# Kernel optimization log

Hardware: AMD Instinct MI355X
Metric: run time of the kernel (lower is better)

Reference implementation:

```python
import jax, jax.numpy as jnp
import numpy as np

B, S, D, H, HZ = 4096, 64, 9, 128, 32
DT = 0.1


def _lstm_cell(x, h, c, Wih, Whh, bih, bhh):
    gates = x @ Wih.T + bih + h @ Whh.T + bhh
    i, f, g, o = jnp.split(gates, 4, axis=-1)
    c_new = jax.nn.sigmoid(f) * c + jax.nn.sigmoid(i) * jnp.tanh(g)
    h_new = jax.nn.sigmoid(o) * jnp.tanh(c_new)
    return h_new, c_new


def _forward(input_batch, W_ih_enc, W_hh_enc, b_ih_enc, b_hh_enc, W_e, V_e, v_e,
             W_d, V_d, v_d, W_ih_dec, W_hh_dec, b_ih_dec, b_hh_dec,
             W_out, b_out, scaler_mean, scaler_std, pos_mean):
    bsz = input_batch.shape[0]
    # ---- encoder with input attention ----
    x_perm = jnp.swapaxes(input_batch, 1, 2)          # (B, D, S)
    attn_input = jnp.einsum('bds,ts->bdt', x_perm, V_e)  # V_e * x^i, precomputed once
    h0 = jnp.zeros((bsz, H), input_batch.dtype)
    c0 = jnp.zeros((bsz, H), input_batch.dtype)

    def enc_step(carry, x_t):
        h, c = carry
        attn_hidden = jnp.concatenate([h, c], axis=1) @ W_e.T          # (B, S)
        comb = jnp.tanh(attn_hidden[:, None, :] + attn_input)          # (B, D, S)
        e = comb @ v_e                                                 # (B, D)
        alpha = jax.nn.softmax(e, axis=1)
        h, c = _lstm_cell(alpha * x_t, h, c, W_ih_enc, W_hh_enc, b_ih_enc, b_hh_enc)
        return (h, c), h

    (h_enc, c_enc), hs = jax.lax.scan(enc_step, (h0, c0), jnp.swapaxes(input_batch, 0, 1))
    enc_hidden = jnp.swapaxes(hs, 0, 1)               # (B, S, H)
    attn_encoder = enc_hidden @ V_d.T                 # V_d * h_j, precomputed once

    # ---- initial physics state ----
    pos = input_batch[:, -1, :3] + pos_mean
    vel = input_batch[:, -1, 3:6] * scaler_std + scaler_mean
    pre_vel = input_batch[:, -2, 3:6] * scaler_std + scaler_mean
    acc = (vel - pre_vel) / DT

    def dec_step(carry, _):
        d, c, pos, vel, acc = carry
        attn_dec = jnp.concatenate([d, c], axis=1) @ W_d.T             # (B, H)
        comb = jnp.tanh(attn_dec[:, None, :] + attn_encoder)           # (B, S, H)
        beta = jax.nn.softmax(comb @ v_d, axis=1)                      # (B, S)
        context = jnp.einsum('bs,bsh->bh', beta, enc_hidden)           # (B, H)
        phys = jnp.concatenate([pos - pos_mean,
                                (vel - scaler_mean) / scaler_std,
                                acc / scaler_std], axis=1)             # (B, 9)
        d, c = _lstm_cell(jnp.concatenate([phys, context], axis=1), d, c,
                          W_ih_dec, W_hh_dec, b_ih_dec, b_hh_dec)
        pred_acc = (jnp.concatenate([d, context], axis=1) @ W_out.T + b_out) * scaler_std
        pos_pred = pos + vel * DT + 0.5 * acc * DT * DT                # Verlet position
        vel_new = vel + 0.5 * (acc + pred_acc) * DT                    # Verlet velocity
        out = jnp.concatenate([pos_pred, vel_new, pred_acc], axis=1)   # (B, 9)
        return (d, c, pos_pred, vel_new, pred_acc), out

    _, outs = jax.lax.scan(dec_step, (h_enc, c_enc, pos, vel, acc), None, length=HZ)
    return jnp.swapaxes(outs, 0, 1)                   # (B, HZ, 9)


def setup_inputs() -> dict:
    key = jax.random.key(0)
    ks = jax.random.split(key, 16)
    p = lambda k, shape, s=0.05: jax.random.normal(k, shape, dtype=jnp.float32) * s
    return dict(
        input_batch=jax.random.normal(ks[0], (B, S, D), dtype=jnp.float32),
        W_ih_enc=p(ks[1], (4 * H, D)), W_hh_enc=p(ks[2], (4 * H, H)),
        b_ih_enc=jnp.zeros((4 * H,), jnp.float32), b_hh_enc=jnp.zeros((4 * H,), jnp.float32),
        W_e=p(ks[3], (S, 2 * H)), V_e=p(ks[4], (S, S)), v_e=p(ks[5], (S,)),
        W_d=p(ks[6], (H, 2 * H)), V_d=p(ks[7], (H, H)), v_d=p(ks[8], (H,)),
        W_ih_dec=p(ks[9], (4 * H, 9 + H)), W_hh_dec=p(ks[10], (4 * H, H)),
        b_ih_dec=jnp.zeros((4 * H,), jnp.float32), b_hh_dec=jnp.zeros((4 * H,), jnp.float32),
        W_out=p(ks[11], (3, 2 * H)), b_out=jnp.zeros((3,), jnp.float32),
        scaler_mean=p(ks[12], (3,), 0.1),
        scaler_std=jnp.abs(p(ks[13], (3,), 0.1)) + 1.0,
        pos_mean=p(ks[14], (3,), 0.1),
    )


def reference(input_batch, W_ih_enc, W_hh_enc, b_ih_enc, b_hh_enc, W_e, V_e, v_e,
              W_d, V_d, v_d, W_ih_dec, W_hh_dec, b_ih_dec, b_hh_dec,
              W_out, b_out, scaler_mean, scaler_std, pos_mean):
    return _forward(input_batch, W_ih_enc, W_hh_enc, b_ih_enc, b_hh_enc, W_e, V_e, v_e,
                    W_d, V_d, v_d, W_ih_dec, W_hh_dec, b_ih_dec, b_hh_dec,
                    W_out, b_out, scaler_mean, scaler_std, pos_mean)
```

## Files before the change

### kernel.cpp

```cpp
#include <hip/hip_runtime.h>
#include <hip/hip_bf16.h>
#include <hip/hip_fp8.h>

#define B_   4096
#define S_   64
#define D_   9
#define H_   128
#define HZ_  32
#define DT_  0.1f

#define OFF_WET    0
#define OFF_VET    16384
#define OFF_WENCT  20480
#define OFF_BENC   90624
#define OFF_WDT    91136
#define OFF_WDECT  123904
#define OFF_BDEC   259584
#define OFF_WOUTT  260096
#define OFF_VDT    260864
#define OFF_DECD   277248
#define OFF_DECC   801536
#define F32_TOTAL  1325824
#define PREP_N     277248

#define DCX_S   552
#define OF_D0   0
#define OF_D1   128
#define OF_C    256
#define OF_CTX  384
#define OF_PH   512

typedef __bf16 bf16x8 __attribute__((ext_vector_type(8)));
typedef float  f32x4  __attribute__((ext_vector_type(4)));
typedef float  f32x2  __attribute__((ext_vector_type(2)));

__device__ __forceinline__ float fast_tanh(float x) {
    float e = __expf(2.0f * x);
    return 1.0f - __fdividef(2.0f, e + 1.0f);
}
__device__ __forceinline__ float sigf(float x) {
    return __fdividef(1.0f, 1.0f + __expf(-x));
}
__device__ __forceinline__ float bf_lo(unsigned int u) { return __uint_as_float(u << 16); }
__device__ __forceinline__ float bf_hi(unsigned int u) { return __uint_as_float(u & 0xffff0000u); }
__device__ __forceinline__ float bfu2f(unsigned short u) { return __uint_as_float((unsigned int)u << 16); }
__device__ __forceinline__ unsigned short f2bfu(float f) {
    __hip_bfloat16 b = __float2bfloat16(f);
    return *(unsigned short*)&b;
}
__device__ __forceinline__ unsigned int pack_bf(float lo, float hi) {
    return (unsigned int)f2bfu(lo) | ((unsigned int)f2bfu(hi) << 16);
}
__device__ __forceinline__ float f8tof(unsigned int byte) {
    __hip_fp8_e4m3 t; t.__x = (unsigned char)byte; return (float)t;
}
__device__ __forceinline__ unsigned char f2f8(float f) {
    __hip_fp8_e4m3 q(f); return q.__x;
}
__device__ __forceinline__ unsigned int pack4_f8(float a, float b, float c, float d) {
    return (unsigned int)f2f8(a) | ((unsigned int)f2f8(b) << 8) |
           ((unsigned int)f2f8(c) << 16) | ((unsigned int)f2f8(d) << 24);
}
template<bool HI>
__device__ __forceinline__ f32x2 cvt2f8(unsigned int u) {
    return __builtin_amdgcn_cvt_pk_f32_fp8(u, HI);
}

__global__ void prep_kernel(const float* __restrict__ Wih_e, const float* __restrict__ Whh_e,
    const float* __restrict__ bih_e, const float* __restrict__ bhh_e,
    const float* __restrict__ W_e, const float* __restrict__ V_e,
    const float* __restrict__ W_d, const float* __restrict__ V_d,
    const float* __restrict__ Wih_d, const float* __restrict__ Whh_d,
    const float* __restrict__ bih_d, const float* __restrict__ bhh_d,
    const float* __restrict__ W_out, float* __restrict__ ws) {
  for (int idx = blockIdx.x * blockDim.x + threadIdx.x; idx < PREP_N;
       idx += gridDim.x * blockDim.x) {
    int i = idx;
    if (i < 16384) { continue; }
    i -= 16384;
    if (i < 4096) { int s = i >> 6, t = i & 63; ws[OFF_VET + i] = V_e[t * 64 + s]; continue; }
    i -= 4096;
    if (i < 70144) { continue; }
    i -= 70144;
    if (i < 512) { ws[OFF_BENC + i] = bih_e[i] + bhh_e[i]; continue; }
    i -= 512;
    if (i < 32768) { continue; }
    i -= 32768;
    if (i < 135680) { continue; }
    i -= 135680;
    if (i < 512) { ws[OFF_BDEC + i] = bih_d[i] + bhh_d[i]; continue; }
    i -= 512;
    if (i < 768) { int k = i / 3, j = i % 3; ws[OFF_WOUTT + i] = W_out[j * 256 + k]; continue; }
  }
}

__global__ void prep_mfma_kernel(const float* __restrict__ W_d,
    const float* __restrict__ Wih_d, const float* __restrict__ Whh_d,
    unsigned short* __restrict__ WdTm, unsigned short* __restrict__ WdecTm) {
  int idx = blockIdx.x * blockDim.x + threadIdx.x;
  if (idx < 32768) {
    int j = idx & 7, l = (idx >> 3) & 63, t = idx >> 9;
    int nt = t & 7, ks = t >> 3;
    int k = ks * 32 + (l >> 4) * 8 + j;
    int n = nt * 16 + (l & 15);
    WdTm[idx] = f2bfu(W_d[n * 256 + k]);
    return;
  }
  int i2 = idx - 32768;
  if (i2 < 147456) {
    int j = i2 & 7, l = (i2 >> 3) & 63, t = i2 >> 9;
    int ks = t % 9, tile = t / 9;
    int q = tile & 3, is = tile >> 2;
    int k = ks * 32 + (l >> 4) * 8 + j;
    int g = q * 128 + is * 16 + (l & 15);
    float v;
    if (k < 128)      v = Whh_d[g * 128 + k];
    else if (k < 256) v = Wih_d[g * 137 + 9 + (k - 128)];
    else if (k < 265) v = Wih_d[g * 137 + (k - 256)];
    else              v = 0.f;
    WdecTm[i2] = f2bfu(v);
  }
}

__global__ void prep_enc_mfma_kernel(const float* __restrict__ W_e,
    const float* __restrict__ Wih_e, const float* __restrict__ Whh_e,
    const float* __restrict__ V_d,
    unsigned short* __restrict__ WeTm, unsigned short* __restrict__ WencTm,
    unsigned short* __restrict__ VdTm) {
  int idx = blockIdx.x * blockDim.x + threadIdx.x;
  if (idx < 16384) {
    int j = idx & 7, l = (idx >> 3) & 63, tile = idx >> 9;
    int nt = tile & 3, ks = tile >> 2;
    int k = ks * 32 + (l >> 4) * 8 + j;
    int n = nt * 16 + (l & 15);
    WeTm[idx] = f2bfu(W_e[n * 256 + k]);
    return;
  }
  int i2 = idx - 16384;
  if (i2 < 81920) {
    int j = i2 & 7, l = (i2 >> 3) & 63, tile = i2 >> 9;
    int ks = tile % 5, tq = tile / 5;
    int q = tq & 3, is = tq >> 2;
    int kk = (l >> 4) * 8 + j;
    int g = q * 128 + is * 16 + (l & 15);
    float v;
    if (ks < 4) v = Whh_e[g * 128 + ks * 32 + kk];
    else        v = (kk < 9) ? Wih_e[g * 9 + kk] : 0.f;
    WencTm[i2] = f2bfu(v);
    return;
  }
  int i3 = i2 - 81920;
  if (i3 < 16384) {
    int j = i3 & 7, l = (i3 >> 3) & 63, tile = i3 >> 9;
    int nt = tile & 7, ks = tile >> 3;
    int i = ks * 32 + (l >> 4) * 8 + j;
    int n = nt * 16 + (l & 15);
    VdTm[i3] = f2bfu(V_d[n * 128 + i]);
  }
}

__global__ __launch_bounds__(512, 1) void encoder_mfma_kernel(
    const float* __restrict__ x_in, const float* __restrict__ ws,
    const float* __restrict__ v_e_g,
    const unsigned short* __restrict__ WeTm, const unsigned short* __restrict__ WencTm,
    __hip_bfloat16* __restrict__ EH,
    unsigned short* __restrict__ dG, float* __restrict__ cG) {
  __shared__ unsigned short hA[2][16 * 296];
  __shared__ float cF[16 * 132];
  __shared__ float ahL[16 * 64];
  __shared__ unsigned short aiL[16 * 576];
  __shared__ unsigned short xbL[16 * 576];

  const int tid = threadIdx.x;
  const int b0 = blockIdx.x * 16;
  const int l = tid & 63, w = tid >> 6;
  const int quad = l >> 4, l15 = l & 15;

  for (int i = tid; i < 16 * 576; i += 512) {
    int m = i / 576, r = i % 576;
    xbL[i] = f2bfu(x_in[(size_t)(b0 + m) * 576 + r]);
  }
  for (int i = tid; i < 2 * 16 * 296; i += 512) ((unsigned short*)hA)[i] = 0;
  for (int i = tid; i < 16 * 132; i += 512) cF[i] = 0.f;
  __syncthreads();

  {
    const float* __restrict__ VeT = ws + OFF_VET;
    for (int i = tid; i < 16 * 576; i += 512) {
      int t = i & 63, dd = (i >> 6) % 9, m = i / 576;
      float acc = 0.f;
      for (int s = 0; s < 64; ++s) acc += bfu2f(xbL[m * 576 + s * 9 + dd]) * VeT[s * 64 + t];
      aiL[m * 576 + dd * 64 + t] = f2bfu(acc);
    }
  }
  const float ve_r = v_e_g[l];
  const int ig = w * 16 + l15;
  float bbq[4];
  #pragma unroll
  for (int q = 0; q < 4; ++q) bbq[q] = ws[OFF_BENC + q * 128 + ig];
  __syncthreads();

  for (int t = 0; t < S_; ++t) {
    unsigned short* bufC = hA[t & 1];
    unsigned short* bufN = hA[(t + 1) & 1];
    if (w < 4) {
      f32x4 acc = {0.f, 0.f, 0.f, 0.f};
      #pragma unroll
      for (int ks = 0; ks < 8; ++ks) {
        uint4 au = *(const uint4*)&bufC[l15 * 296 + ks * 32 + quad * 8];
        uint4 bu = *(const uint4*)(WeTm + (size_t)((ks * 4 + w) * 64 + l) * 8);
        acc = __builtin_amdgcn_mfma_f32_16x16x32_bf16(
            __builtin_bit_cast(bf16x8, au), __builtin_bit_cast(bf16x8, bu), acc, 0, 0, 0);
      }
      #pragma unroll
      for (int r = 0; r < 4; ++r)
        ahL[(quad * 4 + r) * 64 + w * 16 + l15] = acc[r];
    }
    __syncthreads();
    {
      const int m0 = 2 * w, m1 = 2 * w + 1;
      float a0 = ahL[m0 * 64 + l], a1 = ahL[m1 * 64 + l];
      float e0k = -1e30f, e1k = -1e30f;
      #pragma unroll
      for (int dd = 0; dd < 9; ++dd) {
        float t0 = fast_tanh(a0 + bfu2f(aiL[m0 * 576 + dd * 64 + l])) * ve_r;
        float t1 = fast_tanh(a1 + bfu2f(aiL[m1 * 576 + dd * 64 + l])) * ve_r;
        #pragma unroll
        for (int off = 32; off; off >>= 1) {
          t0 += __shfl_xor(t0, off, 64);
          t1 += __shfl_xor(t1, off, 64);
        }
        if (l == dd) { e0k = t0; e1k = t1; }
      }
      float mx0 = e0k, mx1 = e1k;
      #pragma unroll
      for (int off = 8; off; off >>= 1) {
        mx0 = fmaxf(mx0, __shfl_xor(mx0, off, 64));
        mx1 = fmaxf(mx1, __shfl_xor(mx1, off, 64));
      }
      float ex0 = (l < 9) ? __expf(e0k - mx0) : 0.f;
      float ex1 = (l < 9) ? __expf(e1k - mx1) : 0.f;
      float s0 = ex0, s1 = ex1;
      #pragma unroll
      for (int off = 8; off; off >>= 1) {
        s0 += __shfl_xor(s0, off, 64);
        s1 += __shfl_xor(s1, off, 64);
      }
      if (l < 9) {
        bufC[m0 * 296 + 256 + l] = f2bfu(__fdividef(ex0, s0) * bfu2f(xbL[m0 * 576 + t * 9 + l]));
        bufC[m1 * 296 + 256 + l] = f2bfu(__fdividef(ex1, s1) * bfu2f(xbL[m1 * 576 + t * 9 + l]));
      }
    }
    __syncthreads();
    {
      uint4 af[5];
      #pragma unroll
      for (int ks = 0; ks < 4; ++ks)
        af[ks] = *(const uint4*)&bufC[l15 * 296 + ks * 32 + quad * 8];
      af[4] = *(const uint4*)&bufC[l15 * 296 + 256 + quad * 8];
      f32x4 g4[4];
      #pragma unroll
      for (int q = 0; q < 4; ++q) {
        f32x4 acc = {0.f, 0.f, 0.f, 0.f};
        #pragma unroll
        for (int ks = 0; ks < 5; ++ks) {
          uint4 bu = *(const uint4*)(WencTm + (size_t)(((w * 4 + q) * 5 + ks) * 64 + l) * 8);
          acc = __builtin_amdgcn_mfma_f32_16x16x32_bf16(
              __builtin_bit_cast(bf16x8, af[ks]), __builtin_bit_cast(bf16x8, bu), acc, 0, 0, 0);
        }
        g4[q] = acc;
      }
      #pragma unroll
      for (int r = 0; r < 4; ++r) {
        int m = quad * 4 + r;
        float gi = g4[0][r] + bbq[0];
        float gf = g4[1][r] + bbq[1];
        float gg = g4[2][r] + bbq[2];
        float go = g4[3][r] + bbq[3];
        float co = cF[m * 132 + ig];
        float cn = sigf(gf) * co + sigf(gi) * fast_tanh(gg);
        float hn = sigf(go) * fast_tanh(cn);
        cF[m * 132 + ig] = cn;
        bufN[m * 296 + ig] = f2bfu(hn);
        bufN[m * 296 + 128 + ig] = f2bfu(cn);
        EH[((size_t)(b0 + m) * S_ + t) * H_ + ig] = __float2bfloat16(hn);
      }
    }
    __syncthreads();
  }
  for (int i = tid; i < 16 * 128; i += 512) {
    int m = i >> 7, ii = i & 127;
    dG[(size_t)(b0 + m) * 128 + ii] = hA[0][m * 296 + ii];
    cG[(size_t)(b0 + m) * 128 + ii] = cF[m * 132 + ii];
  }
}

__global__ __launch_bounds__(256) void attnenc_mfma_kernel(
    const unsigned short* __restrict__ EH, const unsigned short* __restrict__ VdTm,
    unsigned char* __restrict__ AETf8, unsigned char* __restrict__ EHf8) {
  const int tid = threadIdx.x;
  const int b = blockIdx.x * 4 + (tid >> 6);
  const int l = tid & 63;
  const int quad = l >> 4, l15 = l & 15;

  const unsigned short* ehb = EH + (size_t)b * 8192;
  uint4 A[4][4];
  #pragma unroll
  for (int st = 0; st < 4; ++st)
    #pragma unroll
    for (int ks = 0; ks < 4; ++ks)
      A[st][ks] = *(const uint4*)(ehb + (st * 16 + l15) * 128 + ks * 32 + quad * 8);

  {
    unsigned char* e8b = EHf8 + (size_t)b * 8192;
    #pragma unroll
    for (int st = 0; st < 4; ++st)
      #pragma unroll
      for (int ks = 0; ks < 4; ++ks) {
        uint4 a = A[st][ks];
        uint2 pk;
        pk.x = pack4_f8(bf_lo(a.x), bf_hi(a.x), bf_lo(a.y), bf_hi(a.y));
        pk.y = pack4_f8(bf_lo(a.z), bf_hi(a.z), bf_lo(a.w), bf_hi(a.w));
        *(uint2*)(e8b + (st * 16 + l15) * 128 + ks * 32 + quad * 8) = pk;
      }
  }

  unsigned char* outb = AETf8 + (size_t)b * 8192;
  const int k = l15;
  #pragma unroll
  for (int nt = 0; nt < 8; ++nt) {
    uint4 Bf[4];
    #pragma unroll
    for (int ks = 0; ks < 4; ++ks)
      Bf[ks] = *(const uint4*)(VdTm + (size_t)((ks * 8 + nt) * 64 + l) * 8);
    int kg = nt * 16 + k;
    int kb = kg >> 3, k7 = kg & 7;
    #pragma unroll
    for (int st = 0; st < 4; ++st) {
      f32x4 acc = {0.f, 0.f, 0.f, 0.f};
      #pragma unroll
      for (int ks = 0; ks < 4; ++ks)
        acc = __builtin_amdgcn_mfma_f32_16x16x32_bf16(
            __builtin_bit_cast(bf16x8, A[st][ks]), __builtin_bit_cast(bf16x8, Bf[ks]), acc, 0, 0, 0);
      #pragma unroll
      for (int r = 0; r < 4; ++r) {
        int s = st * 16 + quad * 4 + r;
        outb[kb * 512 + s * 8 + k7] = f2f8(acc[r]);
      }
    }
  }
}

__global__ __launch_bounds__(512, 2) void dec_fused_kernel(
    const float* __restrict__ ws,
    const unsigned char* __restrict__ AETf8, const unsigned char* __restrict__ EHf8,
    const unsigned short* __restrict__ dG, const float* __restrict__ cG,
    const unsigned short* __restrict__ WdTm, const unsigned short* __restrict__ WdecTm,
    const float* __restrict__ v_d_g, const float* __restrict__ b_out_g,
    const float* __restrict__ smean_g, const float* __restrict__ sstd_g,
    const float* __restrict__ pmean_g,
    const float* __restrict__ x_in,
    float* __restrict__ out) {
  __shared__ unsigned char  AET[8][8192];
  __shared__ unsigned char  EHL[8][8192];
  __shared__ unsigned short dcx[16 * DCX_S];
  __shared__ unsigned short adL[8 * 128];
  __shared__ float          bet[8][64];
  __shared__ float          vdL[128];
  __shared__ float          pcs[8 * 3 * 8];
  __shared__ float          pvs[8 * 12];

  const int tid = threadIdx.x;
  const int b0 = blockIdx.x * 8;
  const int l = tid & 63, w = tid >> 6;
  const int quad = l >> 4, l15 = l & 15;
  const int i = w * 16 + l15;

  for (int idx = tid; idx < 16 * DCX_S; idx += 512) dcx[idx] = 0;
  {
    const uint4* srcA = (const uint4*)(AETf8 + (size_t)b0 * 8192);
    const uint4* srcE = (const uint4*)(EHf8 + (size_t)b0 * 8192);
    uint4* dstA = (uint4*)AET;
    uint4* dstE = (uint4*)EHL;
    for (int idx = tid; idx < 4096; idx += 512) {
      dstA[idx] = srcA[idx];
      dstE[idx] = srcE[idx];
    }
  }
  if (tid < 128) vdL[tid] = v_d_g[tid];
  __syncthreads();

  if (tid < 128) {
    int m = tid >> 4, i0 = (tid & 15) * 8;
    uint4 dv = *(const uint4*)(dG + (size_t)(b0 + m) * 128 + i0);
    *(uint4*)&dcx[m * DCX_S + OF_D0 + i0] = dv;
    float4 c0 = *(const float4*)(cG + (size_t)(b0 + m) * 128 + i0);
    float4 c1 = *(const float4*)(cG + (size_t)(b0 + m) * 128 + i0 + 4);
    uint4 pk;
    pk.x = pack_bf(c0.x, c0.y); pk.y = pack_bf(c0.z, c0.w);
    pk.z = pack_bf(c1.x, c1.y); pk.w = pack_bf(c1.z, c1.w);
    *(uint4*)&dcx[m * DCX_S + OF_C + i0] = pk;
  }
  if (tid < 24) {
    int m = tid / 3, jj = tid % 3;
    const float* xi = x_in + (size_t)(b0 + m) * 576;
    float sm = smean_g[jj], ss = sstd_g[jj], pm = pmean_g[jj];
    float v  = xi[63 * 9 + 3 + jj] * ss + sm;
    float pv = xi[62 * 9 + 3 + jj] * ss + sm;
    float pos = xi[63 * 9 + jj] + pm;
    float ac = (v - pv) / DT_;
    float* P = pvs + m * 12;
    P[jj] = pos; P[3 + jj] = v; P[6 + jj] = ac;
    dcx[m * DCX_S + OF_PH + jj]     = f2bfu(pos - pm);
    dcx[m * DCX_S + OF_PH + 3 + jj] = f2bfu((v - sm) / ss);
    dcx[m * DCX_S + OF_PH + 6 + jj] = f2bfu(ac / ss);
  }
  float bb[4];
  #pragma unroll
  for (int q = 0; q < 4; ++q) bb[q] = ws[OFF_BDEC + q * 128 + i];
  float k_sm = 0.f, k_ss = 1.f, k_pm = 0.f, k_bo = 0.f;
  if (tid < 24) {
    int jj = tid % 3;
    k_sm = smean_g[jj]; k_ss = sstd_g[jj]; k_pm = pmean_g[jj]; k_bo = b_out_g[jj];
  }
  float cReg[4];
  #pragma unroll
  for (int r = 0; r < 4; ++r)
    cReg[r] = (quad < 2) ? cG[(size_t)(b0 + quad * 4 + r) * 128 + i] : 0.f;
  __syncthreads();

  {
    const int nt = w;
    f32x4 acc = {0.f, 0.f, 0.f, 0.f};
    #pragma unroll
    for (int ks = 0; ks < 8; ++ks) {
      int off = (ks < 4) ? (OF_D0 + ks * 32) : (OF_C + (ks - 4) * 32);
      uint4 au = *(const uint4*)&dcx[l15 * DCX_S + off + quad * 8];
      uint4 bu = *(const uint4*)(WdTm + (size_t)((ks * 8 + nt) * 64 + l) * 8);
      acc = __builtin_amdgcn_mfma_f32_16x16x32_bf16(
          __builtin_bit_cast(bf16x8, au), __builtin_bit_cast(bf16x8, bu), acc, 0, 0, 0);
    }
    if (quad < 2) {
      int n = nt * 16 + l15;
      #pragma unroll
      for (int r = 0; r < 4; ++r) adL[(quad * 4 + r) * 128 + n] = f2bfu(acc[r]);
    }
  }
  __syncthreads();

  for (int hz = 0; hz < HZ_; ++hz) {
    const int dcur = (hz & 1) ? OF_D1 : OF_D0;
    const int dnxt = (hz & 1) ? OF_D0 : OF_D1;

    {
      const unsigned char* aet = AET[w];
      const unsigned short* adp = adL + w * 128;
      float eacc[4] = {0.f, 0.f, 0.f, 0.f};
      #pragma unroll
      for (int kb = 0; kb < 16; ++kb) {
        uint2 av = *(const uint2*)(aet + kb * 512 + l * 8);
        uint4 ad8 = *(const uint4*)(adp + kb * 8);
        float4 v0 = *(const float4*)&vdL[kb * 8];
        float4 v1 = *(const float4*)&vdL[kb * 8 + 4];
        f32x2 p0 = cvt2f8<false>(av.x), p1 = cvt2f8<true>(av.x);
        f32x2 p2 = cvt2f8<false>(av.y), p3 = cvt2f8<true>(av.y);
        float e = eacc[kb & 3];
        e += fast_tanh(bf_lo(ad8.x) + p0[0]) * v0.x;
        e += fast_tanh(bf_hi(ad8.x) + p0[1]) * v0.y;
        e += fast_tanh(bf_lo(ad8.y) + p1[0]) * v0.z;
        e += fast_tanh(bf_hi(ad8.y) + p1[1]) * v0.w;
        e += fast_tanh(bf_lo(ad8.z) + p2[0]) * v1.x;
        e += fast_tanh(bf_hi(ad8.z) + p2[1]) * v1.y;
        e += fast_tanh(bf_lo(ad8.w) + p3[0]) * v1.z;
        e += fast_tanh(bf_hi(ad8.w) + p3[1]) * v1.w;
        eacc[kb & 3] = e;
      }
      float e0 = (eacc[0] + eacc[1]) + (eacc[2] + eacc[3]);
      float mx = e0;
      #pragma unroll
      for (int off = 32; off; off >>= 1) mx = fmaxf(mx, __shfl_xor(mx, off, 64));
      float ex = __expf(e0 - mx);
      float ss = ex;
      #pragma unroll
      for (int off = 32; off; off >>= 1) ss += __shfl_xor(ss, off, 64);
      bet[w][l] = __fdividef(ex, ss);
    }
    {
      const unsigned char* ehb = EHL[w];
      const int i0 = l15 * 8;
      float a[8];
      #pragma unroll
      for (int r = 0; r < 8; ++r) a[r] = 0.f;
      #pragma unroll
      for (int it = 0; it < 16; ++it) {
        int s = quad * 16 + it;
        uint2 ev = *(const uint2*)(ehb + s * 128 + i0);
        float bt = bet[w][s];
        f32x2 c0 = cvt2f8<false>(ev.x), c1 = cvt2f8<true>(ev.x);
        f32x2 c2 = cvt2f8<false>(ev.y), c3 = cvt2f8<true>(ev.y);
        a[0] += bt * c0[0]; a[1] += bt * c0[1];
        a[2] += bt * c1[0]; a[3] += bt * c1[1];
        a[4] += bt * c2[0]; a[5] += bt * c2[1];
        a[6] += bt * c3[0]; a[7] += bt * c3[1];
      }
      #pragma unroll
      for (int r = 0; r < 8; ++r) {
        a[r] += __shfl_xor(a[r], 16, 64);
        a[r] += __shfl_xor(a[r], 32, 64);
      }
      if (quad == 0) {
        uint4 pk;
        pk.x = pack_bf(a[0], a[1]); pk.y = pack_bf(a[2], a[3]);
        pk.z = pack_bf(a[4], a[5]); pk.w = pack_bf(a[6], a[7]);
        *(uint4*)&dcx[w * DCX_S + OF_CTX + i0] = pk;
      }
    }
    __syncthreads();

    {
      f32x4 g4[4];
      #pragma unroll
      for (int q = 0; q < 4; ++q) g4[q] = (f32x4){0.f, 0.f, 0.f, 0.f};
      #pragma unroll
      for (int ks = 0; ks < 9; ++ks) {
        int off = (ks < 4) ? (dcur + ks * 32)
                           : ((ks < 8) ? (OF_CTX + (ks - 4) * 32) : OF_PH);
        uint4 af = *(const uint4*)&dcx[l15 * DCX_S + off + quad * 8];
        #pragma unroll
        for (int q = 0; q < 4; ++q) {
          uint4 bu = *(const uint4*)(WdecTm + (size_t)(((w * 4 + q) * 9 + ks) * 64 + l) * 8);
          g4[q] = __builtin_amdgcn_mfma_f32_16x16x32_bf16(
              __builtin_bit_cast(bf16x8, af), __builtin_bit_cast(bf16x8, bu), g4[q], 0, 0, 0);
        }
      }
      if (quad < 2) {
        #pragma unroll
        for (int r = 0; r < 4; ++r) {
          int m = quad * 4 + r;
          float gi = g4[0][r] + bb[0];
          float gf = g4[1][r] + bb[1];
          float gg = g4[2][r] + bb[2];
          float go = g4[3][r] + bb[3];
          float cn = sigf(gf) * cReg[r] + sigf(gi) * fast_tanh(gg);
          float hn = sigf(go) * fast_tanh(cn);
          cReg[r] = cn;
          dcx[m * DCX_S + dnxt + i] = f2bfu(hn);
          dcx[m * DCX_S + OF_C + i] = f2bfu(cn);
        }
      }
    }
    __syncthreads();

    {
      const int nt = w;
      f32x4 acc = {0.f, 0.f, 0.f, 0.f};
      #pragma unroll
      for (int ks = 0; ks < 8; ++ks) {
        int off = (ks < 4) ? (dnxt + ks * 32) : (OF_C + (ks - 4) * 32);
        uint4 au = *(const uint4*)&dcx[l15 * DCX_S + off + quad * 8];
        uint4 bu = *(const uint4*)(WdTm + (size_t)((ks * 8 + nt) * 64 + l) * 8);
        acc = __builtin_amdgcn_mfma_f32_16x16x32_bf16(
            __builtin_bit_cast(bf16x8, au), __builtin_bit_cast(bf16x8, bu), acc, 0, 0, 0);
      }
      if (quad < 2) {
        int n = nt * 16 + l15;
        #pragma unroll
        for (int r = 0; r < 4; ++r) adL[(quad * 4 + r) * 128 + n] = f2bfu(acc[r]);
      }
    }
    if (tid < 192) {
      int m = tid / 24, r2 = tid % 24, jj = r2 >> 3, part = r2 & 7;
      int kbase = (part < 4) ? (dnxt + part * 32) : (OF_CTX + (part - 4) * 32);
      float acc = 0.f;
      #pragma unroll 4
      for (int kk = 0; kk < 32; ++kk)
        acc += bfu2f(dcx[m * DCX_S + kbase + kk]) * ws[OFF_WOUTT + (part * 32 + kk) * 3 + jj];
      pcs[(m * 3 + jj) * 8 + part] = acc;
    }
    __syncthreads();

    if (tid < 24) {
      int m = tid / 3, jj = tid % 3;
      float s = k_bo;
      #pragma unroll
      for (int p = 0; p < 8; ++p) s += pcs[(m * 3 + jj) * 8 + p];
      float pacc = s * k_ss;
      float* P = pvs + m * 12;
      float pos = P[jj], vel = P[3 + jj], ac = P[6 + jj];
      float ppred = pos + vel * DT_ + 0.5f * ac * DT_ * DT_;
      float vnew  = vel + 0.5f * (ac + pacc) * DT_;
      size_t ob = ((size_t)(b0 + m) * HZ_ + hz) * 9;
      out[ob + jj] = ppred; out[ob + 3 + jj] = vnew; out[ob + 6 + jj] = pacc;
      P[jj] = ppred; P[3 + jj] = vnew; P[6 + jj] = pacc;
      dcx[m * DCX_S + OF_PH + jj]     = f2bfu(ppred - k_pm);
      dcx[m * DCX_S + OF_PH + 3 + jj] = f2bfu((vnew - k_sm) / k_ss);
      dcx[m * DCX_S + OF_PH + 6 + jj] = f2bfu(pacc / k_ss);
    }
  }
}

extern "C" void kernel_launch(void* const* d_in, const int* in_sizes, int n_in,
                              void* d_out, int out_size, void* d_ws, size_t ws_size,
                              hipStream_t stream) {
  (void)in_sizes; (void)n_in; (void)out_size; (void)ws_size;
  const float* x      = (const float*)d_in[0];
  const float* Wih_e  = (const float*)d_in[1];
  const float* Whh_e  = (const float*)d_in[2];
  const float* bih_e  = (const float*)d_in[3];
  const float* bhh_e  = (const float*)d_in[4];
  const float* W_e    = (const float*)d_in[5];
  const float* V_e    = (const float*)d_in[6];
  const float* v_e    = (const float*)d_in[7];
  const float* W_d    = (const float*)d_in[8];
  const float* V_d    = (const float*)d_in[9];
  const float* v_d    = (const float*)d_in[10];
  const float* Wih_d  = (const float*)d_in[11];
  const float* Whh_d  = (const float*)d_in[12];
  const float* bih_d  = (const float*)d_in[13];
  const float* bhh_d  = (const float*)d_in[14];
  const float* W_out  = (const float*)d_in[15];
  const float* b_out  = (const float*)d_in[16];
  const float* smean  = (const float*)d_in[17];
  const float* sstd   = (const float*)d_in[18];
  const float* pmean  = (const float*)d_in[19];

  float* ws = (float*)d_ws;
  unsigned short* WeTm   = (unsigned short*)(ws + OFF_WET);
  unsigned short* WencTm = (unsigned short*)(ws + OFF_WENCT);
  unsigned short* WdTm   = (unsigned short*)(ws + OFF_WDT);
  unsigned short* WdecTm = (unsigned short*)(ws + OFF_WDECT);
  unsigned short* VdTm   = (unsigned short*)(ws + OFF_VDT);
  unsigned short* dG     = (unsigned short*)(ws + OFF_DECD);
  float* cG = ws + OFF_DECC;
  unsigned short* ub  = (unsigned short*)(ws + F32_TOTAL);
  unsigned short* EH  = ub;
  unsigned char*  AETf8 = (unsigned char*)(ub + 33554432);
  unsigned char*  EHf8  = AETf8 + (size_t)B_ * 8192;
  float* out = (float*)d_out;

  prep_kernel<<<(PREP_N + 255) / 256, 256, 0, stream>>>(
      Wih_e, Whh_e, bih_e, bhh_e, W_e, V_e, W_d, V_d,
      Wih_d, Whh_d, bih_d, bhh_d, W_out, ws);
  prep_mfma_kernel<<<(32768 + 147456 + 255) / 256, 256, 0, stream>>>(
      W_d, Wih_d, Whh_d, WdTm, WdecTm);
  prep_enc_mfma_kernel<<<(16384 + 81920 + 16384 + 255) / 256, 256, 0, stream>>>(
      W_e, Wih_e, Whh_e, V_d, WeTm, WencTm, VdTm);
  encoder_mfma_kernel<<<B_ / 16, 512, 0, stream>>>(
      x, ws, v_e, WeTm, WencTm, (__hip_bfloat16*)EH, dG, cG);
  attnenc_mfma_kernel<<<B_ / 4, 256, 0, stream>>>(EH, VdTm, AETf8, EHf8);
  dec_fused_kernel<<<B_ / 8, 512, 0, stream>>>(
      ws, AETf8, EHf8, dG, cG, WdTm, WdecTm,
      v_d, b_out, smean, sstd, pmean, x, out);
}
```

Before: 1.995 ms.

## Shrink decoder blocks to 4 rows and restructure tanh attention math

Rebatches the fused decoder kernel to 4 batch rows per 256-thread block instead of 8 per 512, with each wave covering two gate tiles. This halves per-block shared memory and uses less padding in the MFMA A operand. It also folds the tanh into a single exp/rcp term by pre-scaling attention activations by 2/ln2 and rewriting v·tanh as a constant plus -2v/(1+e). Outputs are staged in LDS and written out coalesced at the end. The risks are fp8 precision loss from the pre-scaling and that the MFMA M-dimension is now only a quarter used.

Result: slower. 2.477 ms (+24.2%).

```diff
diff --git a/kernel.cpp b/kernel.cpp
--- a/kernel.cpp
+++ b/kernel.cpp
@@ -23,12 +23,20 @@
 #define F32_TOTAL  1325824
 #define PREP_N     277248
 
-#define DCX_S   552
+#define DCX_S   544
 #define OF_D0   0
 #define OF_D1   128
 #define OF_C    256
 #define OF_CTX  384
 #define OF_PH   512
+#define AL_ADL  2176
+#define AL_BET  3200
+#define AL_M2V  3712
+#define AL_PCS  3968
+#define AL_PVS  4160
+#define AL_OUT  4256
+
+#define KC 2.885390081777927f
 
 typedef __bf16 bf16x8 __attribute__((ext_vector_type(8)));
 typedef float  f32x4  __attribute__((ext_vector_type(4)));
@@ -64,6 +72,12 @@
 template<bool HI>
 __device__ __forceinline__ f32x2 cvt2f8(unsigned int u) {
     return __builtin_amdgcn_cvt_pk_f32_fp8(u, HI);
+}
+__device__ __forceinline__ float tanh_term(float x, float m2v, float acc) {
+    float E; asm("v_exp_f32 %0, %1" : "=v"(E) : "v"(x));
+    float D = E + 1.0f;
+    float R; asm("v_rcp_f32 %0, %1" : "=v"(R) : "v"(D));
+    return __builtin_fmaf(m2v, R, acc);
 }
 
 __global__ void prep_kernel(const float* __restrict__ Wih_e, const float* __restrict__ Whh_e,
@@ -345,13 +359,13 @@
       #pragma unroll
       for (int r = 0; r < 4; ++r) {
         int s = st * 16 + quad * 4 + r;
-        outb[kb * 512 + s * 8 + k7] = f2f8(acc[r]);
-      }
-    }
-  }
-}
-
-__global__ __launch_bounds__(512, 2) void dec_fused_kernel(
+        outb[kb * 512 + s * 8 + k7] = f2f8(acc[r] * KC);
+      }
+    }
+  }
+}
+
+__global__ __launch_bounds__(256, 2) void dec_fused_kernel(
     const float* __restrict__ ws,
     const unsigned char* __restrict__ AETf8, const unsigned char* __restrict__ EHf8,
     const unsigned short* __restrict__ dG, const float* __restrict__ cG,
@@ -361,36 +375,37 @@
     const float* __restrict__ pmean_g,
     const float* __restrict__ x_in,
     float* __restrict__ out) {
-  __shared__ unsigned char  AET[8][8192];
-  __shared__ unsigned char  EHL[8][8192];
-  __shared__ unsigned short dcx[16 * DCX_S];
-  __shared__ unsigned short adL[8 * 128];
-  __shared__ float          bet[8][64];
-  __shared__ float          vdL[128];
-  __shared__ float          pcs[8 * 3 * 8];
-  __shared__ float          pvs[8 * 12];
+  __shared__ __align__(16) unsigned short dcx[15 * DCX_S];
+  __shared__ __align__(16) unsigned char  AET[4][8192];
+  __shared__ __align__(16) unsigned char  EHL[4][8192];
+
+  float* adLf = (float*)&dcx[AL_ADL];
+  float* bet  = (float*)&dcx[AL_BET];
+  float* m2vL = (float*)&dcx[AL_M2V];
+  float* pcs  = (float*)&dcx[AL_PCS];
+  float* pvs  = (float*)&dcx[AL_PVS];
+  float* outB = (float*)&dcx[AL_OUT];
 
   const int tid = threadIdx.x;
-  const int b0 = blockIdx.x * 8;
+  const int b0 = blockIdx.x * 4;
   const int l = tid & 63, w = tid >> 6;
   const int quad = l >> 4, l15 = l & 15;
-  const int i = w * 16 + l15;
-
-  for (int idx = tid; idx < 16 * DCX_S; idx += 512) dcx[idx] = 0;
+
+  for (int idx = tid; idx < 15 * DCX_S; idx += 256) dcx[idx] = 0;
   {
     const uint4* srcA = (const uint4*)(AETf8 + (size_t)b0 * 8192);
     const uint4* srcE = (const uint4*)(EHf8 + (size_t)b0 * 8192);
     uint4* dstA = (uint4*)AET;
     uint4* dstE = (uint4*)EHL;
-    for (int idx = tid; idx < 4096; idx += 512) {
+    for (int idx = tid; idx < 2048; idx += 256) {
       dstA[idx] = srcA[idx];
       dstE[idx] = srcE[idx];
     }
   }
-  if (tid < 128) vdL[tid] = v_d_g[tid];
   __syncthreads();
 
-  if (tid < 128) {
+  if (tid < 128) m2vL[tid] = -2.0f * v_d_g[tid];
+  if (tid < 64) {
     int m = tid >> 4, i0 = (tid & 15) * 8;
     uint4 dv = *(const uint4*)(dG + (size_t)(b0 + m) * 128 + i0);
     *(uint4*)&dcx[m * DCX_S + OF_D0 + i0] = dv;
@@ -401,7 +416,7 @@
     pk.z = pack_bf(c1.x, c1.y); pk.w = pack_bf(c1.z, c1.w);
     *(uint4*)&dcx[m * DCX_S + OF_C + i0] = pk;
   }
-  if (tid < 24) {
+  if (tid < 12) {
     int m = tid / 3, jj = tid % 3;
     const float* xi = x_in + (size_t)(b0 + m) * 576;
     float sm = smean_g[jj], ss = sstd_g[jj], pm = pmean_g[jj];
@@ -415,22 +430,36 @@
     dcx[m * DCX_S + OF_PH + 3 + jj] = f2bfu((v - sm) / ss);
     dcx[m * DCX_S + OF_PH + 6 + jj] = f2bfu(ac / ss);
   }
-  float bb[4];
+  float bb[2][4];
   #pragma unroll
-  for (int q = 0; q < 4; ++q) bb[q] = ws[OFF_BDEC + q * 128 + i];
+  for (int t2 = 0; t2 < 2; ++t2) {
+    int i2 = (w + 4 * t2) * 16 + l15;
+    #pragma unroll
+    for (int q = 0; q < 4; ++q) bb[t2][q] = ws[OFF_BDEC + q * 128 + i2];
+  }
   float k_sm = 0.f, k_ss = 1.f, k_pm = 0.f, k_bo = 0.f;
-  if (tid < 24) {
+  if (tid < 12) {
     int jj = tid % 3;
     k_sm = smean_g[jj]; k_ss = sstd_g[jj]; k_pm = pmean_g[jj]; k_bo = b_out_g[jj];
   }
-  float cReg[4];
+  float cReg[2][4];
   #pragma unroll
-  for (int r = 0; r < 4; ++r)
-    cReg[r] = (quad < 2) ? cG[(size_t)(b0 + quad * 4 + r) * 128 + i] : 0.f;
+  for (int t2 = 0; t2 < 2; ++t2)
+    #pragma unroll
+    for (int r = 0; r < 4; ++r)
+      cReg[t2][r] = (quad == 0)
+          ? cG[(size_t)(b0 + r) * 128 + (w + 4 * t2) * 16 + l15] : 0.f;
   __syncthreads();
 
-  {
-    const int nt = w;
+  float S_v = 0.f;
+  for (int k2 = 0; k2 < 128; k2 += 4) {
+    float4 mv = *(const float4*)&m2vL[k2];
+    S_v -= 0.5f * ((mv.x + mv.y) + (mv.z + mv.w));
+  }
+
+  #pragma unroll
+  for (int t2 = 0; t2 < 2; ++t2) {
+    const int nt = w + 4 * t2;
     f32x4 acc = {0.f, 0.f, 0.f, 0.f};
     #pragma unroll
     for (int ks = 0; ks < 8; ++ks) {
@@ -440,10 +469,10 @@
       acc = __builtin_amdgcn_mfma_f32_16x16x32_bf16(
           __builtin_bit_cast(bf16x8, au), __builtin_bit_cast(bf16x8, bu), acc, 0, 0, 0);
     }
-    if (quad < 2) {
+    if (quad == 0) {
       int n = nt * 16 + l15;
       #pragma unroll
-      for (int r = 0; r < 4; ++r) adL[(quad * 4 + r) * 128 + n] = f2bfu(acc[r]);
+      for (int r = 0; r < 4; ++r) adLf[r * 128 + n] = acc[r] * KC;
     }
   }
   __syncthreads();
@@ -454,25 +483,26 @@
 
     {
       const unsigned char* aet = AET[w];
-      const unsigned short* adp = adL + w * 128;
-      float eacc[4] = {0.f, 0.f, 0.f, 0.f};
+      const float* adf = adLf + w * 128;
+      float eacc[4] = {S_v, 0.f, 0.f, 0.f};
       #pragma unroll
       for (int kb = 0; kb < 16; ++kb) {
         uint2 av = *(const uint2*)(aet + kb * 512 + l * 8);
-        uint4 ad8 = *(const uint4*)(adp + kb * 8);
-        float4 v0 = *(const float4*)&vdL[kb * 8];
-        float4 v1 = *(const float4*)&vdL[kb * 8 + 4];
+        float4 a0 = *(const float4*)(adf + kb * 8);
+        float4 a1 = *(const float4*)(adf + kb * 8 + 4);
+        float4 m0 = *(const float4*)(m2vL + kb * 8);
+        float4 m1 = *(const float4*)(m2vL + kb * 8 + 4);
         f32x2 p0 = cvt2f8<false>(av.x), p1 = cvt2f8<true>(av.x);
         f32x2 p2 = cvt2f8<false>(av.y), p3 = cvt2f8<true>(av.y);
         float e = eacc[kb & 3];
-        e += fast_tanh(bf_lo(ad8.x) + p0[0]) * v0.x;
-        e += fast_tanh(bf_hi(ad8.x) + p0[1]) * v0.y;
-        e += fast_tanh(bf_lo(ad8.y) + p1[0]) * v0.z;
-        e += fast_tanh(bf_hi(ad8.y) + p1[1]) * v0.w;
-        e += fast_tanh(bf_lo(ad8.z) + p2[0]) * v1.x;
-        e += fast_tanh(bf_hi(ad8.z) + p2[1]) * v1.y;
-        e += fast_tanh(bf_lo(ad8.w) + p3[0]) * v1.z;
-        e += fast_tanh(bf_hi(ad8.w) + p3[1]) * v1.w;
+        e = tanh_term(a0.x + p0[0], m0.x, e);
+        e = tanh_term(a0.y + p0[1], m0.y, e);
+        e = tanh_term(a0.z + p1[0], m0.z, e);
+        e = tanh_term(a0.w + p1[1], m0.w, e);
+        e = tanh_term(a1.x + p2[0], m1.x, e);
+        e = tanh_term(a1.y + p2[1], m1.y, e);
+        e = tanh_term(a1.z + p3[0], m1.z, e);
+        e = tanh_term(a1.w + p3[1], m1.w, e);
         eacc[kb & 3] = e;
       }
       float e0 = (eacc[0] + eacc[1]) + (eacc[2] + eacc[3]);
@@ -483,7 +513,7 @@
       float ss = ex;
       #pragma unroll
       for (int off = 32; off; off >>= 1) ss += __shfl_xor(ss, off, 64);
-      bet[w][l] = __fdividef(ex, ss);
+      bet[w * 64 + l] = __fdividef(ex, ss);
     }
     {
       const unsigned char* ehb = EHL[w];
@@ -495,7 +525,7 @@
       for (int it = 0; it < 16; ++it) {
         int s = quad * 16 + it;
         uint2 ev = *(const uint2*)(ehb + s * 128 + i0);
-        float bt = bet[w][s];
+        float bt = bet[w * 64 + s];
         f32x2 c0 = cvt2f8<false>(ev.x), c1 = cvt2f8<true>(ev.x);
         f32x2 c2 = cvt2f8<false>(ev.y), c3 = cvt2f8<true>(ev.y);
         a[0] += bt * c0[0]; a[1] += bt * c0[1];
@@ -518,41 +548,51 @@
     __syncthreads();
 
     {
-      f32x4 g4[4];
-      #pragma unroll
-      for (int q = 0; q < 4; ++q) g4[q] = (f32x4){0.f, 0.f, 0.f, 0.f};
+      f32x4 g4[2][4];
+      #pragma unroll
+      for (int t2 = 0; t2 < 2; ++t2)
+        #pragma unroll
+        for (int q = 0; q < 4; ++q) g4[t2][q] = (f32x4){0.f, 0.f, 0.f, 0.f};
       #pragma unroll
       for (int ks = 0; ks < 9; ++ks) {
         int off = (ks < 4) ? (dcur + ks * 32)
                            : ((ks < 8) ? (OF_CTX + (ks - 4) * 32) : OF_PH);
         uint4 af = *(const uint4*)&dcx[l15 * DCX_S + off + quad * 8];
         #pragma unroll
-        for (int q = 0; q < 4; ++q) {
-          uint4 bu = *(const uint4*)(WdecTm + (size_t)(((w * 4 + q) * 9 + ks) * 64 + l) * 8);
-          g4[q] = __builtin_amdgcn_mfma_f32_16x16x32_bf16(
-              __builtin_bit_cast(bf16x8, af), __builtin_bit_cast(bf16x8, bu), g4[q], 0, 0, 0);
+        for (int t2 = 0; t2 < 2; ++t2) {
+          const int is = w + 4 * t2;
+          #pragma unroll
+          for (int q = 0; q < 4; ++q) {
+            uint4 bu = *(const uint4*)(WdecTm + (size_t)(((is * 4 + q) * 9 + ks) * 64 + l) * 8);
+            g4[t2][q] = __builtin_amdgcn_mfma_f32_16x16x32_bf16(
+                __builtin_bit_cast(bf16x8, af), __builtin_bit_cast(bf16x8, bu), g4[t2][q], 0, 0, 0);
+          }
         }
       }
-      if (quad < 2) {
+      if (quad == 0) {
         #pragma unroll
-        for (int r = 0; r < 4; ++r) {
-          int m = quad * 4 + r;
-          float gi = g4[0][r] + bb[0];
-          float gf = g4[1][r] + bb[1];
-          float gg = g4[2][r] + bb[2];
-          float go = g4[3][r] + bb[3];
-          float cn = sigf(gf) * cReg[r] + sigf(gi) * fast_tanh(gg);
-          float hn = sigf(go) * fast_tanh(cn);
-          cReg[r] = cn;
-          dcx[m * DCX_S + dnxt + i] = f2bfu(hn);
-          dcx[m * DCX_S + OF_C + i] = f2bfu(cn);
+        for (int t2 = 0; t2 < 2; ++t2) {
+          const int i2 = (w + 4 * t2) * 16 + l15;
+          #pragma unroll
+          for (int r = 0; r < 4; ++r) {
+            float gi = g4[t2][0][r] + bb[t2][0];
+            float gf = g4[t2][1][r] + bb[t2][1];
+            float gg = g4[t2][2][r] + bb[t2][2];
+            float go = g4[t2][3][r] + bb[t2][3];
+            float cn = sigf(gf) * cReg[t2][r] + sigf(gi) * fast_tanh(gg);
+            float hn = sigf(go) * fast_tanh(cn);
+            cReg[t2][r] = cn;
+            dcx[r * DCX_S + dnxt + i2] = f2bfu(hn);
+            dcx[r * DCX_S + OF_C + i2] = f2bfu(cn);
+          }
         }
       }
     }
     __syncthreads();
 
-    {
-      const int nt = w;
+    #pragma unroll
+    for (int t2 = 0; t2 < 2; ++t2) {
+      const int nt = w + 4 * t2;
       f32x4 acc = {0.f, 0.f, 0.f, 0.f};
       #pragma unroll
       for (int ks = 0; ks < 8; ++ks) {
@@ -562,13 +602,13 @@
         acc = __builtin_amdgcn_mfma_f32_16x16x32_bf16(
             __builtin_bit_cast(bf16x8, au), __builtin_bit_cast(bf16x8, bu), acc, 0, 0, 0);
       }
-      if (quad < 2) {
+      if (quad == 0) {
         int n = nt * 16 + l15;
         #pragma unroll
-        for (int r = 0; r < 4; ++r) adL[(quad * 4 + r) * 128 + n] = f2bfu(acc[r]);
-      }
-    }
-    if (tid < 192) {
+        for (int r = 0; r < 4; ++r) adLf[r * 128 + n] = acc[r] * KC;
+      }
+    }
+    if (tid < 96) {
       int m = tid / 24, r2 = tid % 24, jj = r2 >> 3, part = r2 & 7;
       int kbase = (part < 4) ? (dnxt + part * 32) : (OF_CTX + (part - 4) * 32);
       float acc = 0.f;
@@ -579,7 +619,7 @@
     }
     __syncthreads();
 
-    if (tid < 24) {
+    if (tid < 12) {
       int m = tid / 3, jj = tid % 3;
       float s = k_bo;
       #pragma unroll
@@ -589,14 +629,17 @@
       float pos = P[jj], vel = P[3 + jj], ac = P[6 + jj];
       float ppred = pos + vel * DT_ + 0.5f * ac * DT_ * DT_;
       float vnew  = vel + 0.5f * (ac + pacc) * DT_;
-      size_t ob = ((size_t)(b0 + m) * HZ_ + hz) * 9;
-      out[ob + jj] = ppred; out[ob + 3 + jj] = vnew; out[ob + 6 + jj] = pacc;
+      float* OB = outB + (m * 32 + hz) * 9;
+      OB[jj] = ppred; OB[3 + jj] = vnew; OB[6 + jj] = pacc;
       P[jj] = ppred; P[3 + jj] = vnew; P[6 + jj] = pacc;
       dcx[m * DCX_S + OF_PH + jj]     = f2bfu(ppred - k_pm);
       dcx[m * DCX_S + OF_PH + 3 + jj] = f2bfu((vnew - k_sm) / k_ss);
       dcx[m * DCX_S + OF_PH + 6 + jj] = f2bfu(pacc / k_ss);
     }
   }
+  __syncthreads();
+  for (int idx = tid; idx < 1152; idx += 256)
+    out[(size_t)b0 * 288 + idx] = outB[idx];
 }
 
 extern "C" void kernel_launch(void* const* d_in, const int* in_sizes, int n_in,
@@ -648,7 +691,7 @@
   encoder_mfma_kernel<<<B_ / 16, 512, 0, stream>>>(
       x, ws, v_e, WeTm, WencTm, (__hip_bfloat16*)EH, dG, cG);
   attnenc_mfma_kernel<<<B_ / 4, 256, 0, stream>>>(EH, VdTm, AETf8, EHf8);
-  dec_fused_kernel<<<B_ / 8, 512, 0, stream>>>(
+  dec_fused_kernel<<<B_ / 4, 256, 0, stream>>>(
       ws, AETf8, EHf8, dG, cG, WdTm, WdecTm,
       v_d, b_out, smean, sstd, pmean, x, out);
 }
```
